# Optimization experiments

Measured on AMD Instinct MI355X. Metric: run time of the kernel, lower is better.

## Reference

```python
import jax, jax.numpy as jnp
import numpy as np
from functools import partial

N = 50000      # nodes
E = 800000     # edges
B = 64         # graphs in batch
D = 64         # embedding_dim (= per-head out_dim)
H = 2          # num_heads
G = 50         # n_gaussians
HID = 128      # hidden_dim of edge-filter net
MLP_DIM = 128  # mlp_dim of OutputMLP
OUT = 1        # output_dim
L = 3          # n_interactions
CUTOFF = 8.0
MEAN = 0.0
STD = 1.0


def ssp(x):
    # shifted softplus: softplus(x) - log(2)
    return jax.nn.softplus(x) - jnp.log(2.0)


def setup_inputs() -> dict:
    key = jax.random.key(0)
    ks = jax.random.split(key, 24)
    R = jax.random.normal(ks[0], (N, 3), dtype=jnp.float32) * 3.0
    Z = jax.random.randint(ks[1], (N,), 0, 100)
    src = jax.random.randint(ks[2], (E,), 0, N)
    dst = jax.random.randint(ks[3], (E,), 0, N)
    graph_ids = jnp.sort(jax.random.randint(ks[4], (N,), 0, B))
    # embedding table with padding_idx=0 zeroed
    emb_table = (jax.random.normal(ks[5], (100, D), dtype=jnp.float32) * 0.1).at[0].set(0.0)
    offsets = jnp.linspace(0.0, CUTOFF, G, dtype=jnp.float32)
    widths = jnp.full((G,), offsets[1] - offsets[0], dtype=jnp.float32)
    s = 0.1
    rn = lambda k, shp: jax.random.normal(k, shp, dtype=jnp.float32) * s
    return {
        "R": R, "Z": Z, "src": src, "dst": dst, "graph_ids": graph_ids,
        "emb_table": emb_table, "offsets": offsets, "widths": widths,
        "fc_w": rn(ks[6], (L, D, H * D)),
        "attn_l": rn(ks[7], (L, H, D)),
        "attn_r": rn(ks[8], (L, H, D)),
        "filt_w1": rn(ks[9], (L, G, HID)), "filt_b1": jnp.zeros((L, HID), jnp.float32),
        "filt_w2": rn(ks[10], (L, HID, H * D)), "filt_b2": jnp.zeros((L, H * D), jnp.float32),
        "mlp_w1": rn(ks[11], (L, H * D, D)), "mlp_b1": jnp.zeros((L, D), jnp.float32),
        "mlp_w2": rn(ks[12], (L, D, D)), "mlp_b2": jnp.zeros((L, D), jnp.float32),
        "out_w1": rn(ks[13], (D, MLP_DIM)), "out_b1": jnp.zeros((MLP_DIM,), jnp.float32),
        "out_w2": rn(ks[14], (MLP_DIM, OUT)), "out_b2": jnp.zeros((OUT,), jnp.float32),
    }


def _forward(R, emb_table, offsets, widths, fc_w, attn_l, attn_r,
             filt_w1, filt_b1, filt_w2, filt_b2,
             mlp_w1, mlp_b1, mlp_w2, mlp_b2,
             out_w1, out_b1, out_w2, out_b2,
             Z, src, dst, graph_ids):
    # per-edge distances
    r = jnp.linalg.norm(R[src] - R[dst], axis=1)  # (E,)
    # Gaussian smearing (trainable offsets/widths, schnetpack style)
    coeff = -0.5 / (widths ** 2)
    gs = jnp.exp(coeff * (r[:, None] - offsets) ** 2)  # (E, G)
    # cosine cutoff
    C = 0.5 * (jnp.cos(r * (jnp.pi / CUTOFF)) + 1.0) * (r < CUTOFF).astype(r.dtype)  # (E,)
    x = emb_table[Z]  # (N, D)
    for l in range(L):
        h = (x @ fc_w[l]).reshape(N, H, D)  # (N, H, D)
        # cfconv-style edge filter from gaussian features
        w = ssp(gs @ filt_w1[l] + filt_b1[l]) @ filt_w2[l] + filt_b2[l]  # (E, H*D)
        w = w.reshape(E, H, D)
        msg = h[src] * w * C[:, None, None]  # (E, H, D)
        # GAT attention, softmax over incoming edges per dst node
        el = jnp.einsum('nhd,hd->nh', h, attn_l[l])
        er = jnp.einsum('nhd,hd->nh', h, attn_r[l])
        e = jax.nn.leaky_relu(el[src] + er[dst], negative_slope=0.2)  # (E, H)
        m = jax.ops.segment_max(e, dst, num_segments=N)  # (N, H)
        ex = jnp.exp(e - m[dst])
        denom = jax.ops.segment_sum(ex, dst, num_segments=N)  # (N, H)
        alpha = ex / denom[dst]  # (E, H)
        agg = jax.ops.segment_sum(alpha[:, :, None] * msg, dst, num_segments=N)  # (N, H, D)
        v = ssp(agg).reshape(N, H * D)
        v = ssp(v @ mlp_w1[l] + mlp_b1[l]) @ mlp_w2[l] + mlp_b2[l]  # (N, D)
        x = x + v
    hh = ssp(x @ out_w1 + out_b1) @ out_w2 + out_b2  # (N, OUT)
    hh = hh * STD + MEAN
    return jax.ops.segment_sum(hh, graph_ids, num_segments=B)  # (B, OUT)


def reference(R, Z, src, dst, graph_ids, emb_table, offsets, widths,
              fc_w, attn_l, attn_r, filt_w1, filt_b1, filt_w2, filt_b2,
              mlp_w1, mlp_b1, mlp_w2, mlp_b2,
              out_w1, out_b1, out_w2, out_b2):
    return _forward(R, emb_table, offsets, widths, fc_w, attn_l, attn_r,
                    filt_w1, filt_b1, filt_w2, filt_b2,
                    mlp_w1, mlp_b1, mlp_w2, mlp_b2,
                    out_w1, out_b1, out_w2, out_b2,
                    Z, src, dst, graph_ids)
```

## Files before the change

kernel.cpp:

```cpp
#include <hip/hip_runtime.h>
#include <stdint.h>

#define N_NODES 50000
#define N_EDGES 800000
#define B_GRAPHS 64
#define D_DIM 64
#define HD 128
#define G_GAUSS 50
#define HID_DIM 128
#define L_LAYERS 3
#define LN2 0.69314718055994530942f
#define PI_OVER_8 0.39269908169872414f
#define NCHUNK 196

#define TN 64
#define TLD 132
#define XLD 68
#define NBLK ((N_NODES + TN - 1) / TN)

#define LUT_T 2048
#define LUT_ROWS (LUT_T + 1)
#define LROWS 8

__device__ __forceinline__ float sspf(float x) {
    float ax = fabsf(x);
    return fmaxf(x, 0.f) + __logf(1.f + __expf(-ax)) - LN2;
}
__device__ __forceinline__ unsigned short f2bf(float f) {
    union { float f; unsigned int i; } v; v.f = f;
    unsigned int u = v.i;
    return (unsigned short)((u + 0x7FFFu + ((u >> 16) & 1u)) >> 16);
}

__global__ void repr_prep(int* __restrict__ count, float* __restrict__ dout) {
    int i = blockIdx.x * 256 + threadIdx.x;
    if (i < N_NODES) count[i] = 0;
    else if (i < N_NODES + B_GRAPHS) dout[i - N_NODES] = 0.f;
}

#define ZTOT ((N_NODES * HD + 2 * N_NODES) / 4)
__global__ void repr_zero(float* __restrict__ agg, float* __restrict__ denom) {
    int i = blockIdx.x * 256 + threadIdx.x;
    float4 z = make_float4(0.f, 0.f, 0.f, 0.f);
    if (i < N_NODES * HD / 4) ((float4*)agg)[i] = z;
    else if (i < ZTOT) ((float4*)denom)[i - N_NODES * HD / 4] = z;
}

__global__ __launch_bounds__(256) void repr_lut_build(
    const float* __restrict__ offs, const float* __restrict__ widths,
    const float* __restrict__ fw1, const float* __restrict__ fb1,
    const float* __restrict__ fw2, const float* __restrict__ fb2,
    unsigned int* __restrict__ lut)
{
    __shared__ float gs_s[LROWS + 1][G_GAUSS];
    __shared__ float hid_s[LROWS + 1][HID_DIM];
    __shared__ float wc_s[LROWS + 1][HD];
    const int nb = LUT_T / LROWS;
    int l = blockIdx.x / nb;
    int i0r = (blockIdx.x % nb) * LROWS;
    int tid = threadIdx.x;
    const float step = 8.0f / LUT_T;

    for (int j = tid; j < (LROWS + 1) * G_GAUSS; j += 256) {
        int r = j / G_GAUSS, k = j - r * G_GAUSS;
        float rr = (i0r + r) * step;
        float wdt = widths[k];
        float dr = rr - offs[k];
        gs_s[r][k] = expf(-0.5f / (wdt * wdt) * dr * dr);
    }
    __syncthreads();

    int c = tid & 127, sub = tid >> 7;
    int rlo = sub * 4;
    {
        const float* W1 = fw1 + (size_t)l * G_GAUSS * HID_DIM + c;
        float acc[5];
        float bb = fb1[l * HID_DIM + c];
        #pragma unroll
        for (int r = 0; r < 5; r++) acc[r] = bb;
        for (int k = 0; k < G_GAUSS; k++) {
            float wv = W1[k * HID_DIM];
            #pragma unroll
            for (int r = 0; r < 5; r++)
                acc[r] = fmaf(gs_s[rlo + r][k], wv, acc[r]);
        }
        #pragma unroll
        for (int r = 0; r < 5; r++) hid_s[rlo + r][c] = sspf(acc[r]);
    }
    __syncthreads();
    {
        const float* W2 = fw2 + (size_t)l * HID_DIM * HD + c;
        float acc[5];
        float bb = fb2[l * HD + c];
        #pragma unroll
        for (int r = 0; r < 5; r++) acc[r] = bb;
        for (int k = 0; k < HID_DIM; k++) {
            float wv = W2[k * HD];
            #pragma unroll
            for (int r = 0; r < 5; r++)
                acc[r] = fmaf(hid_s[rlo + r][k], wv, acc[r]);
        }
        #pragma unroll
        for (int r = 0; r < 5; r++) {
            float rr = (i0r + rlo + r) * step;
            float C = (rr < 8.0f) ? 0.5f * (cosf(rr * PI_OVER_8) + 1.f) : 0.f;
            wc_s[rlo + r][c] = acc[r] * C;
        }
    }
    __syncthreads();
    for (int j = tid; j < LROWS * HD; j += 256) {
        int r = j >> 7, cc = j & 127;
        unsigned int lo = f2bf(wc_s[r][cc]);
        unsigned int hi = f2bf(wc_s[r + 1][cc]);
        lut[((size_t)l * LUT_ROWS + i0r + r) * HD + cc] = lo | (hi << 16);
    }
    if (i0r == LUT_T - LROWS && tid < HD)
        lut[((size_t)l * LUT_ROWS + LUT_T) * HD + tid] = 0u;
}

__global__ void repr_hist(const float* __restrict__ R,
                          const int* __restrict__ src, const int* __restrict__ dst,
                          int* __restrict__ count,
                          int2* __restrict__ pk) {
    int e = blockIdx.x * blockDim.x + threadIdx.x;
    if (e >= N_EDGES) return;
    int s = src[e], d = dst[e];
    float dx = R[3*s+0] - R[3*d+0];
    float dy = R[3*s+1] - R[3*d+1];
    float dz = R[3*s+2] - R[3*d+2];
    float r = sqrtf(dx*dx + dy*dy + dz*dz);
    unsigned rf = (r < 8.0f) ? (unsigned)(r * 16777216.f) : (2048u << 16);
    if (rf > (2048u << 16)) rf = 2048u << 16;
    pk[e] = make_int2((int)((unsigned)s | ((unsigned)d << 16)), (int)rf);
    atomicAdd(&count[d], 1);
}

__global__ void repr_scanA(const int* __restrict__ cnt, int* __restrict__ excl,
                           int* __restrict__ bsum) {
    __shared__ int tmp[256];
    int t = threadIdx.x, b = blockIdx.x;
    int i = b * 256 + t;
    int v = (i < N_NODES) ? cnt[i] : 0;
    tmp[t] = v; __syncthreads();
    for (int off = 1; off < 256; off <<= 1) {
        int add = (t >= off) ? tmp[t - off] : 0;
        __syncthreads();
        tmp[t] += add;
        __syncthreads();
    }
    if (i < N_NODES) excl[i] = tmp[t] - v;
    if (t == 255) bsum[b] = tmp[255];
}
__global__ void repr_scanB(const int* __restrict__ bsum, int* __restrict__ bpref) {
    __shared__ int tmp[256];
    int t = threadIdx.x;
    int v = (t < NCHUNK) ? bsum[t] : 0;
    tmp[t] = v; __syncthreads();
    for (int off = 1; off < 256; off <<= 1) {
        int add = (t >= off) ? tmp[t - off] : 0;
        __syncthreads();
        tmp[t] += add;
        __syncthreads();
    }
    if (t < NCHUNK) bpref[t] = tmp[t] - v;
}
__global__ void repr_scanC(const int* __restrict__ excl, const int* __restrict__ bpref,
                           int* __restrict__ cur) {
    int i = blockIdx.x * 256 + threadIdx.x;
    if (i < N_NODES) cur[i] = excl[i] + bpref[blockIdx.x];
}

__global__ void repr_scatter(const int2* __restrict__ pk,
                             int* __restrict__ cur,
                             int2* __restrict__ surv) {
    int e = blockIdx.x * blockDim.x + threadIdx.x;
    if (e >= N_EDGES) return;
    int2 v = pk[e];
    int d = (int)((unsigned)v.x >> 16);
    int pos = atomicAdd(&cur[d], 1);
    surv[pos] = v;
}


__device__ __forceinline__ void load_ssp_agg(int base, int tid,
        const float* __restrict__ agg, const float* __restrict__ denom,
        float* __restrict__ bufA) {
    int row = tid >> 2;
    int c0 = (tid & 3) << 5;
    int n = base + row;
    float2 dn = *(const float2*)&denom[2 * (size_t)n];
    float i0v = dn.x > 0.f ? 1.f / dn.x : 0.f;
    float i1v = dn.y > 0.f ? 1.f / dn.y : 0.f;
    float inv = (c0 < 64) ? i0v : i1v;
    const float* ap = agg + (size_t)n * HD + c0;
    float* tp = bufA + row * TLD + c0;
    #pragma unroll
    for (int j = 0; j < 8; j++) {
        float4 v = *(const float4*)(ap + j * 4);
        tp[j*4+0] = sspf(v.x * inv); tp[j*4+1] = sspf(v.y * inv);
        tp[j*4+2] = sspf(v.z * inv); tp[j*4+3] = sspf(v.w * inv);
    }
}

__device__ __forceinline__ void gemm_mlp(int base, int tid,
        const float* __restrict__ w1, const float* __restrict__ b1,
        const float* __restrict__ w2, const float* __restrict__ b2,
        float* __restrict__ x, float* __restrict__ bufA, float* __restrict__ v1s)
{
    const int rg = tid >> 4, cg = tid & 15;
    const int r0 = rg * 4, c0 = cg * 4;
    float acc[4][4];
    #pragma unroll
    for (int r = 0; r < 4; r++)
        #pragma unroll
        for (int c = 0; c < 4; c++) acc[r][c] = 0.f;
    for (int k0 = 0; k0 < 128; k0 += 4) {
        float av[4][4];
        #pragma unroll
        for (int r = 0; r < 4; r++)
            *(float4*)av[r] = *(const float4*)&bufA[(r0 + r) * TLD + k0];
        #pragma unroll
        for (int kk = 0; kk < 4; kk++) {
            float4 wv = *(const float4*)(w1 + (k0 + kk) * 64 + c0);
            float wf[4] = {wv.x, wv.y, wv.z, wv.w};
            #pragma unroll
            for (int r = 0; r < 4; r++)
                #pragma unroll
                for (int c = 0; c < 4; c++)
                    acc[r][c] = fmaf(av[r][kk], wf[c], acc[r][c]);
        }
    }
    {
        float4 bv = *(const float4*)(b1 + c0);
        float ba[4] = {bv.x, bv.y, bv.z, bv.w};
        #pragma unroll
        for (int r = 0; r < 4; r++)
            #pragma unroll
            for (int c = 0; c < 4; c++)
                v1s[(r0 + r) * XLD + c0 + c] = sspf(acc[r][c] + ba[c]);
    }
    __syncthreads();
    float acc2[4][4];
    #pragma unroll
    for (int r = 0; r < 4; r++)
        #pragma unroll
        for (int c = 0; c < 4; c++) acc2[r][c] = 0.f;
    for (int k0 = 0; k0 < 64; k0 += 4) {
        float av[4][4];
        #pragma unroll
        for (int r = 0; r < 4; r++)
            *(float4*)av[r] = *(const float4*)&v1s[(r0 + r) * XLD + k0];
        #pragma unroll
        for (int kk = 0; kk < 4; kk++) {
            float4 wv = *(const float4*)(w2 + (k0 + kk) * 64 + c0);
            float wf[4] = {wv.x, wv.y, wv.z, wv.w};
            #pragma unroll
            for (int r = 0; r < 4; r++)
                #pragma unroll
                for (int c = 0; c < 4; c++)
                    acc2[r][c] = fmaf(av[r][kk], wf[c], acc2[r][c]);
        }
    }
    {
        float4 bv = *(const float4*)(b2 + c0);
        #pragma unroll
        for (int r = 0; r < 4; r++) {
            int n = base + r0 + r;
            float4 xv = *(const float4*)(x + (size_t)n * 64 + c0);
            float4 o;
            o.x = acc2[r][0] + bv.x + xv.x;
            o.y = acc2[r][1] + bv.y + xv.y;
            o.z = acc2[r][2] + bv.z + xv.z;
            o.w = acc2[r][3] + bv.w + xv.w;
            *(float4*)&bufA[(r0 + r) * XLD + c0] = o;
            if (n < N_NODES) *(float4*)(x + (size_t)n * 64 + c0) = o;
        }
    }
    __syncthreads();
}

__device__ __forceinline__ void gemm_h(int base, int tid,
        const float* __restrict__ bufA,
        const float* __restrict__ fc_w, const float* __restrict__ attn_l,
        const float* __restrict__ attn_r,
        unsigned int* __restrict__ hq, float* __restrict__ el, float* __restrict__ er)
{
    const int rg = tid >> 4, cg = tid & 15;
    const int r0 = rg * 4, c0 = cg * 8;
    float acc[4][8];
    #pragma unroll
    for (int r = 0; r < 4; r++)
        #pragma unroll
        for (int c = 0; c < 8; c++) acc[r][c] = 0.f;
    for (int k0 = 0; k0 < 64; k0 += 4) {
        float av[4][4];
        #pragma unroll
        for (int r = 0; r < 4; r++)
            *(float4*)av[r] = *(const float4*)&bufA[(r0 + r) * XLD + k0];
        #pragma unroll
        for (int kk = 0; kk < 4; kk++) {
            float4 w0 = *(const float4*)(fc_w + (k0 + kk) * 128 + c0);
            float4 w1v = *(const float4*)(fc_w + (k0 + kk) * 128 + c0 + 4);
            float wf[8] = {w0.x, w0.y, w0.z, w0.w, w1v.x, w1v.y, w1v.z, w1v.w};
            #pragma unroll
            for (int r = 0; r < 4; r++)
                #pragma unroll
                for (int c = 0; c < 8; c++)
                    acc[r][c] = fmaf(av[r][kk], wf[c], acc[r][c]);
        }
    }
    float al[8], ar[8];
    #pragma unroll
    for (int c = 0; c < 8; c++) { al[c] = attn_l[c0 + c]; ar[c] = attn_r[c0 + c]; }
    int head = cg >> 3;
    #pragma unroll
    for (int r = 0; r < 4; r++) {
        int n = base + r0 + r;
        float pel = 0.f, per = 0.f;
        #pragma unroll
        for (int c = 0; c < 8; c++) {
            pel = fmaf(acc[r][c], al[c], pel);
            per = fmaf(acc[r][c], ar[c], per);
        }
        if (n < N_NODES) {
            uint4 pv;
            pv.x = (unsigned int)f2bf(acc[r][0]) | ((unsigned int)f2bf(acc[r][1]) << 16);
            pv.y = (unsigned int)f2bf(acc[r][2]) | ((unsigned int)f2bf(acc[r][3]) << 16);
            pv.z = (unsigned int)f2bf(acc[r][4]) | ((unsigned int)f2bf(acc[r][5]) << 16);
            pv.w = (unsigned int)f2bf(acc[r][6]) | ((unsigned int)f2bf(acc[r][7]) << 16);
            *(uint4*)(hq + (size_t)n * 64 + cg * 4) = pv;
        }
        #pragma unroll
        for (int off = 1; off < 8; off <<= 1) {
            pel += __shfl_xor(pel, off, 64);
            per += __shfl_xor(per, off, 64);
        }
        if ((cg & 7) == 0 && n < N_NODES) {
            el[n * 2 + head] = pel;
            er[n * 2 + head] = per;
        }
    }
}

__global__ __launch_bounds__(256) void repr_embed_h(
        const float* __restrict__ emb, const int* __restrict__ Z,
        const float* __restrict__ fc_w, const float* __restrict__ attn_l,
        const float* __restrict__ attn_r,
        float* __restrict__ x, unsigned int* __restrict__ hq,
        float* __restrict__ el, float* __restrict__ er) {
    __shared__ float bufA[TN * XLD];
    int base = blockIdx.x * TN, tid = threadIdx.x;
    int row = tid >> 2;
    int c0 = (tid & 3) << 4;
    int n = base + row;
    int z = (n < N_NODES) ? Z[n] : 0;
    const float* ep = emb + (size_t)z * D_DIM + c0;
    float* bp = bufA + row * XLD + c0;
    #pragma unroll
    for (int j = 0; j < 4; j++) {
        float4 v = *(const float4*)(ep + j * 4);
        *(float4*)(bp + j * 4) = v;
        if (n < N_NODES) *(float4*)(x + (size_t)n * D_DIM + c0 + j * 4) = v;
    }
    __syncthreads();
    gemm_h(base, tid, bufA, fc_w, attn_l, attn_r, hq, el, er);
}

__global__ __launch_bounds__(256) void repr_mlp_h(
        const float* __restrict__ agg, const float* __restrict__ denom,
        const float* __restrict__ w1, const float* __restrict__ b1,
        const float* __restrict__ w2, const float* __restrict__ b2,
        const float* __restrict__ fc_w, const float* __restrict__ attn_l,
        const float* __restrict__ attn_r,
        float* __restrict__ x, unsigned int* __restrict__ hq,
        float* __restrict__ el, float* __restrict__ er) {
    __shared__ float bufA[TN * TLD];
    __shared__ float v1s[TN * XLD];
    int base = blockIdx.x * TN, tid = threadIdx.x;
    load_ssp_agg(base, tid, agg, denom, bufA);
    __syncthreads();
    gemm_mlp(base, tid, w1, b1, w2, b2, x, bufA, v1s);
    gemm_h(base, tid, bufA, fc_w, attn_l, attn_r, hq, el, er);
}

__global__ __launch_bounds__(256) void repr_mlp_out(
        const float* __restrict__ agg, const float* __restrict__ denom,
        const float* __restrict__ w1, const float* __restrict__ b1,
        const float* __restrict__ w2, const float* __restrict__ b2,
        const float* __restrict__ ow1, const float* __restrict__ ob1,
        const float* __restrict__ ow2, const float* __restrict__ ob2,
        float* __restrict__ x, float* __restrict__ hh) {
    __shared__ float bufA[TN * TLD];
    __shared__ float v1s[TN * XLD];
    int base = blockIdx.x * TN, tid = threadIdx.x;
    load_ssp_agg(base, tid, agg, denom, bufA);
    __syncthreads();
    gemm_mlp(base, tid, w1, b1, w2, b2, x, bufA, v1s);
    const int rg = tid >> 4, cg = tid & 15;
    const int r0 = rg * 4, c0 = cg * 8;
    float acc[4][8];
    #pragma unroll
    for (int r = 0; r < 4; r++)
        #pragma unroll
        for (int c = 0; c < 8; c++) acc[r][c] = 0.f;
    for (int k0 = 0; k0 < 64; k0 += 4) {
        float av[4][4];
        #pragma unroll
        for (int r = 0; r < 4; r++)
            *(float4*)av[r] = *(const float4*)&bufA[(r0 + r) * XLD + k0];
        #pragma unroll
        for (int kk = 0; kk < 4; kk++) {
            float4 w0 = *(const float4*)(ow1 + (k0 + kk) * 128 + c0);
            float4 w1v = *(const float4*)(ow1 + (k0 + kk) * 128 + c0 + 4);
            float wf[8] = {w0.x, w0.y, w0.z, w0.w, w1v.x, w1v.y, w1v.z, w1v.w};
            #pragma unroll
            for (int r = 0; r < 4; r++)
                #pragma unroll
                for (int c = 0; c < 8; c++)
                    acc[r][c] = fmaf(av[r][kk], wf[c], acc[r][c]);
        }
    }
    float o1[8], w2c[8];
    #pragma unroll
    for (int c = 0; c < 8; c++) { o1[c] = ob1[c0 + c]; w2c[c] = ow2[c0 + c]; }
    #pragma unroll
    for (int r = 0; r < 4; r++) {
        int n = base + r0 + r;
        float s = 0.f;
        #pragma unroll
        for (int c = 0; c < 8; c++)
            s = fmaf(sspf(acc[r][c] + o1[c]), w2c[c], s);
        #pragma unroll
        for (int off = 1; off < 16; off <<= 1)
            s += __shfl_xor(s, off, 64);
        if (cg == 0 && n < N_NODES) hh[n] = s + ob2[0];
    }
}

#define TILE 64
__global__ __launch_bounds__(256) void repr_msg_lut(
    const int2* __restrict__ surv,
    const float* __restrict__ el, const float* __restrict__ er,
    const unsigned int* __restrict__ hq,
    const unsigned int* __restrict__ lut,
    float* __restrict__ agg, float* __restrict__ denom)
{
    __shared__ int4 rowinfo[TILE];
    __shared__ float scl[TILE][2];
    int base = blockIdx.x * TILE;
    int tid = threadIdx.x;
    int d_own = -1; float e0 = 0.f, e1 = 0.f;
    if (tid < TILE) {
        int2 ev = surv[base + tid];
        int sn = (int)((unsigned)ev.x & 0xFFFFu);
        d_own  = (int)((unsigned)ev.x >> 16);
        unsigned rf = (unsigned)ev.y;
        int i0 = (int)(rf >> 16);
        float fr = (float)(rf & 0xFFFFu) * (1.f / 65536.f);
        float2 a = *(const float2*)&el[2 * sn];
        float2 b = *(const float2*)&er[2 * d_own];
        float v0 = a.x + b.x; v0 = v0 >= 0.f ? v0 : 0.2f * v0;
        float v1 = a.y + b.y; v1 = v1 >= 0.f ? v1 : 0.2f * v1;
        e0 = __expf(v0); e1 = __expf(v1);
        rowinfo[tid] = make_int4(i0, sn, d_own, __float_as_int(fr));
        scl[tid][0] = e0; scl[tid][1] = e1;
    }
    __syncthreads();
    if (tid < TILE) {
        int dprev = __shfl_up(d_own, 1, 64);
        bool headl = (tid == 0) || (d_own != dprev);
        if (headl) {
            float s0 = e0, s1 = e1;
            for (int r = tid + 1; r < TILE; r++) {
                if (rowinfo[r].z != d_own) break;
                s0 += scl[r][0]; s1 += scl[r][1];
            }
            atomicAdd(&denom[2 * d_own], s0);
            atomicAdd(&denom[2 * d_own + 1], s1);
        }
    }
    const int cp = tid & 63;
    const int sp = tid >> 6;
    const int head = cp >> 5;
    const int lo = sp * 16;
    const uint2* __restrict__ l2p = (const uint2*)lut;
    float sum0 = 0.f, sum1 = 0.f;
    int cur_d = -1;
    int seg_first = 1;
    #pragma unroll 4
    for (int j = 0; j < 16; j++) {
        int r = lo + j;
        int4 ri = rowinfo[r];
        if (ri.z != cur_d) {
            if (cur_d >= 0) {
                float* ap = &agg[(size_t)cur_d * HD + 2 * cp];
                if (seg_first) { atomicAdd(ap, sum0); atomicAdd(ap + 1, sum1); }
                else *(float2*)ap = make_float2(sum0, sum1);
            }
            cur_d = ri.z; sum0 = 0.f; sum1 = 0.f; seg_first = (j == 0);
        }
        uint2 tv = l2p[(size_t)ri.x * 64 + cp];
        float fr = __int_as_float(ri.w);
        float wa0 = __uint_as_float(tv.x << 16);
        float wa1 = __uint_as_float(tv.x & 0xFFFF0000u);
        float wb0 = __uint_as_float(tv.y << 16);
        float wb1 = __uint_as_float(tv.y & 0xFFFF0000u);
        unsigned int hv = hq[(size_t)ri.y * 64 + cp];
        float ha = __uint_as_float(hv << 16);
        float hb = __uint_as_float(hv & 0xFFFF0000u);
        float s = scl[r][head];
        float wa = fmaf(fr, wa1 - wa0, wa0);
        float wb = fmaf(fr, wb1 - wb0, wb0);
        sum0 = fmaf(wa * ha, s, sum0);
        sum1 = fmaf(wb * hb, s, sum1);
    }
    if (cur_d >= 0) {
        float* ap = &agg[(size_t)cur_d * HD + 2 * cp];
        atomicAdd(ap, sum0); atomicAdd(ap + 1, sum1);
    }
}

__global__ void repr_gsum(const float* __restrict__ hh, const int* __restrict__ gids,
                          float* __restrict__ dout) {
    __shared__ float bins[B_GRAPHS];
    int t = threadIdx.x;
    if (t < B_GRAPHS) bins[t] = 0.f;
    __syncthreads();
    int i = blockIdx.x * 256 + t;
    if (i < N_NODES) atomicAdd(&bins[gids[i]], hh[i]);
    __syncthreads();
    if (t < B_GRAPHS && bins[t] != 0.f) atomicAdd(&dout[t], bins[t]);
}

extern "C" void kernel_launch(void* const* d_in, const int* in_sizes, int n_in,
                              void* d_out, int out_size, void* d_ws, size_t ws_size,
                              hipStream_t stream) {
    (void)in_sizes; (void)n_in; (void)out_size; (void)ws_size;
    const float* R      = (const float*)d_in[0];
    const int*   Z      = (const int*)d_in[1];
    const int*   src    = (const int*)d_in[2];
    const int*   dst    = (const int*)d_in[3];
    const int*   gids   = (const int*)d_in[4];
    const float* emb    = (const float*)d_in[5];
    const float* offs   = (const float*)d_in[6];
    const float* widths = (const float*)d_in[7];
    const float* fc_w   = (const float*)d_in[8];
    const float* attn_l = (const float*)d_in[9];
    const float* attn_r = (const float*)d_in[10];
    const float* fw1    = (const float*)d_in[11];
    const float* fb1    = (const float*)d_in[12];
    const float* fw2    = (const float*)d_in[13];
    const float* fb2    = (const float*)d_in[14];
    const float* mw1    = (const float*)d_in[15];
    const float* mb1    = (const float*)d_in[16];
    const float* mw2    = (const float*)d_in[17];
    const float* mb2    = (const float*)d_in[18];
    const float* ow1    = (const float*)d_in[19];
    const float* ob1    = (const float*)d_in[20];
    const float* ow2    = (const float*)d_in[21];
    const float* ob2    = (const float*)d_in[22];

    char* p = (char*)d_ws;
    float* x      = (float*)p; p += (size_t)N_NODES * 64 * 4;
    unsigned int* hq = (unsigned int*)p; p += (size_t)N_NODES * 64 * 4;
    float* el     = (float*)p; p += (size_t)N_NODES * 2 * 4;
    float* er     = (float*)p; p += (size_t)N_NODES * 2 * 4;
    float* denom  = (float*)p; p += (size_t)N_NODES * 2 * 4;
    float* agg    = (float*)p; p += (size_t)N_NODES * 128 * 4;
    int2*  surv   = (int2*)p;  p += (size_t)N_EDGES * 8;
    int2*  pk     = (int2*)p;  p += (size_t)N_EDGES * 8;
    float* hh     = (float*)p; p += (size_t)N_NODES * 4;
    int*   bsum   = (int*)p;   p += 1024;
    int*   bpref  = (int*)p;   p += 1024;
    unsigned int* lut = (unsigned int*)pk;
    int* count = (int*)x;
    int* excl  = (int*)((char*)x + 256 * 1024);
    int* cur   = (int*)((char*)x + 512 * 1024);

    repr_prep<<<(N_NODES + B_GRAPHS + 255) / 256, 256, 0, stream>>>(
        count, (float*)d_out);
    repr_hist<<<N_EDGES / 256, 256, 0, stream>>>(R, src, dst, count, pk);
    repr_scanA<<<NCHUNK, 256, 0, stream>>>(count, excl, bsum);
    repr_scanB<<<1, 256, 0, stream>>>(bsum, bpref);
    repr_scanC<<<NCHUNK, 256, 0, stream>>>(excl, bpref, cur);
    repr_scatter<<<N_EDGES / 256, 256, 0, stream>>>(pk, cur, surv);

    repr_lut_build<<<L_LAYERS * (LUT_T / LROWS), 256, 0, stream>>>(
        offs, widths, fw1, fb1, fw2, fb2, lut);

    repr_embed_h<<<NBLK, 256, 0, stream>>>(
        emb, Z, fc_w, attn_l, attn_r, x, hq, el, er);

    for (int l = 0; l < L_LAYERS; l++) {
        repr_zero<<<(ZTOT + 255) / 256, 256, 0, stream>>>(agg, denom);
        repr_msg_lut<<<N_EDGES / TILE, 256, 0, stream>>>(
            surv, el, er, hq, lut + (size_t)l * LUT_ROWS * HD, agg, denom);
        if (l < L_LAYERS - 1) {
            repr_mlp_h<<<NBLK, 256, 0, stream>>>(
                agg, denom, mw1 + (size_t)l * 128 * 64, mb1 + l * 64,
                mw2 + (size_t)l * 64 * 64, mb2 + l * 64,
                fc_w + (size_t)(l + 1) * 64 * 128, attn_l + (l + 1) * 128,
                attn_r + (l + 1) * 128, x, hq, el, er);
        } else {
            repr_mlp_out<<<NBLK, 256, 0, stream>>>(
                agg, denom, mw1 + (size_t)l * 128 * 64, mb1 + l * 64,
                mw2 + (size_t)l * 64 * 64, mb2 + l * 64,
                ow1, ob1, ow2, ob2, x, hh);
        }
    }
    repr_gsum<<<NCHUNK, 256, 0, stream>>>(hh, gids, (float*)d_out);
}
```

Before: 689.6 us.

## Aggregate messages per destination node via CSR rowptr instead of edge tiles

Builds a CSR row pointer from the existing prefix scan and replaces the edge-tiled message kernel with a node-centric kernel. Each block handles 8 destination nodes, with four wave slices striding over each node's incoming edges. Partial sums are reduced in shared memory and written out once per node. This removes the per-layer zeroing kernel and the global atomics on agg and denom, at the cost of load imbalance from variable node degree and serial edge loops.

Measured after the change: 852.9 us. 1.24x slower.

```diff
diff --git a/kernel.cpp b/kernel.cpp
--- a/kernel.cpp
+++ b/kernel.cpp
@@ -36,14 +36,6 @@
     int i = blockIdx.x * 256 + threadIdx.x;
     if (i < N_NODES) count[i] = 0;
     else if (i < N_NODES + B_GRAPHS) dout[i - N_NODES] = 0.f;
-}
-
-#define ZTOT ((N_NODES * HD + 2 * N_NODES) / 4)
-__global__ void repr_zero(float* __restrict__ agg, float* __restrict__ denom) {
-    int i = blockIdx.x * 256 + threadIdx.x;
-    float4 z = make_float4(0.f, 0.f, 0.f, 0.f);
-    if (i < N_NODES * HD / 4) ((float4*)agg)[i] = z;
-    else if (i < ZTOT) ((float4*)denom)[i - N_NODES * HD / 4] = z;
 }
 
 __global__ __launch_bounds__(256) void repr_lut_build(
@@ -165,9 +157,10 @@
     if (t < NCHUNK) bpref[t] = tmp[t] - v;
 }
 __global__ void repr_scanC(const int* __restrict__ excl, const int* __restrict__ bpref,
-                           int* __restrict__ cur) {
+                           int* __restrict__ cur, int* __restrict__ rowptr) {
     int i = blockIdx.x * 256 + threadIdx.x;
-    if (i < N_NODES) cur[i] = excl[i] + bpref[blockIdx.x];
+    if (i < N_NODES) { int v = excl[i] + bpref[blockIdx.x]; cur[i] = v; rowptr[i] = v; }
+    if (i == 0) rowptr[N_NODES] = N_EDGES;
 }
 
 __global__ void repr_scatter(const int2* __restrict__ pk,
@@ -437,87 +430,68 @@
     }
 }
 
-#define TILE 64
-__global__ __launch_bounds__(256) void repr_msg_lut(
-    const int2* __restrict__ surv,
+#define DN 8
+__global__ __launch_bounds__(256) void repr_msg_node(
+    const int2* __restrict__ surv, const int* __restrict__ rowptr,
     const float* __restrict__ el, const float* __restrict__ er,
     const unsigned int* __restrict__ hq,
     const unsigned int* __restrict__ lut,
     float* __restrict__ agg, float* __restrict__ denom)
 {
-    __shared__ int4 rowinfo[TILE];
-    __shared__ float scl[TILE][2];
-    int base = blockIdx.x * TILE;
+    __shared__ float lagg[DN][HD];
+    __shared__ float lden[DN][2];
     int tid = threadIdx.x;
-    int d_own = -1; float e0 = 0.f, e1 = 0.f;
-    if (tid < TILE) {
-        int2 ev = surv[base + tid];
-        int sn = (int)((unsigned)ev.x & 0xFFFFu);
-        d_own  = (int)((unsigned)ev.x >> 16);
-        unsigned rf = (unsigned)ev.y;
-        int i0 = (int)(rf >> 16);
-        float fr = (float)(rf & 0xFFFFu) * (1.f / 65536.f);
-        float2 a = *(const float2*)&el[2 * sn];
-        float2 b = *(const float2*)&er[2 * d_own];
-        float v0 = a.x + b.x; v0 = v0 >= 0.f ? v0 : 0.2f * v0;
-        float v1 = a.y + b.y; v1 = v1 >= 0.f ? v1 : 0.2f * v1;
-        e0 = __expf(v0); e1 = __expf(v1);
-        rowinfo[tid] = make_int4(i0, sn, d_own, __float_as_int(fr));
-        scl[tid][0] = e0; scl[tid][1] = e1;
-    }
-    __syncthreads();
-    if (tid < TILE) {
-        int dprev = __shfl_up(d_own, 1, 64);
-        bool headl = (tid == 0) || (d_own != dprev);
-        if (headl) {
-            float s0 = e0, s1 = e1;
-            for (int r = tid + 1; r < TILE; r++) {
-                if (rowinfo[r].z != d_own) break;
-                s0 += scl[r][0]; s1 += scl[r][1];
-            }
-            atomicAdd(&denom[2 * d_own], s0);
-            atomicAdd(&denom[2 * d_own + 1], s1);
-        }
-    }
-    const int cp = tid & 63;
-    const int sp = tid >> 6;
-    const int head = cp >> 5;
-    const int lo = sp * 16;
+    int cp = tid & 63, slice = tid >> 6;
+    int d0 = blockIdx.x * DN;
+    ((float4*)lagg)[tid] = make_float4(0.f, 0.f, 0.f, 0.f);
+    if (tid < DN * 2) ((float*)lden)[tid] = 0.f;
+    __syncthreads();
+
     const uint2* __restrict__ l2p = (const uint2*)lut;
-    float sum0 = 0.f, sum1 = 0.f;
-    int cur_d = -1;
-    int seg_first = 1;
-    #pragma unroll 4
-    for (int j = 0; j < 16; j++) {
-        int r = lo + j;
-        int4 ri = rowinfo[r];
-        if (ri.z != cur_d) {
-            if (cur_d >= 0) {
-                float* ap = &agg[(size_t)cur_d * HD + 2 * cp];
-                if (seg_first) { atomicAdd(ap, sum0); atomicAdd(ap + 1, sum1); }
-                else *(float2*)ap = make_float2(sum0, sum1);
-            }
-            cur_d = ri.z; sum0 = 0.f; sum1 = 0.f; seg_first = (j == 0);
-        }
-        uint2 tv = l2p[(size_t)ri.x * 64 + cp];
-        float fr = __int_as_float(ri.w);
-        float wa0 = __uint_as_float(tv.x << 16);
-        float wa1 = __uint_as_float(tv.x & 0xFFFF0000u);
-        float wb0 = __uint_as_float(tv.y << 16);
-        float wb1 = __uint_as_float(tv.y & 0xFFFF0000u);
-        unsigned int hv = hq[(size_t)ri.y * 64 + cp];
-        float ha = __uint_as_float(hv << 16);
-        float hb = __uint_as_float(hv & 0xFFFF0000u);
-        float s = scl[r][head];
-        float wa = fmaf(fr, wa1 - wa0, wa0);
-        float wb = fmaf(fr, wb1 - wb0, wb0);
-        sum0 = fmaf(wa * ha, s, sum0);
-        sum1 = fmaf(wb * hb, s, sum1);
-    }
-    if (cur_d >= 0) {
-        float* ap = &agg[(size_t)cur_d * HD + 2 * cp];
-        atomicAdd(ap, sum0); atomicAdd(ap + 1, sum1);
-    }
+    for (int dd = 0; dd < DN; dd++) {
+        int d = d0 + dd;
+        int rs = rowptr[d];
+        int re = rowptr[d + 1];
+        if (rs + slice >= re) continue;
+        float2 b = *(const float2*)&er[2 * d];
+        float acc0 = 0.f, acc1 = 0.f, den0 = 0.f, den1 = 0.f;
+        for (int i = rs + slice; i < re; i += 4) {
+            int2 ev = surv[i];
+            int sn = (int)((unsigned)ev.x & 0xFFFFu);
+            unsigned rf = (unsigned)ev.y;
+            int i0 = (int)(rf >> 16);
+            float fr = (float)(rf & 0xFFFFu) * (1.f / 65536.f);
+            float2 a = *(const float2*)&el[2 * sn];
+            float v0 = a.x + b.x; v0 = v0 >= 0.f ? v0 : 0.2f * v0;
+            float v1 = a.y + b.y; v1 = v1 >= 0.f ? v1 : 0.2f * v1;
+            float e0 = __expf(v0), e1 = __expf(v1);
+            den0 += e0; den1 += e1;
+            uint2 tv = l2p[(size_t)i0 * 64 + cp];
+            unsigned int hv = hq[(size_t)sn * 64 + cp];
+            float wa0 = __uint_as_float(tv.x << 16);
+            float wa1 = __uint_as_float(tv.x & 0xFFFF0000u);
+            float wb0 = __uint_as_float(tv.y << 16);
+            float wb1 = __uint_as_float(tv.y & 0xFFFF0000u);
+            float ha = __uint_as_float(hv << 16);
+            float hb = __uint_as_float(hv & 0xFFFF0000u);
+            float s = (cp < 32) ? e0 : e1;
+            float wa = fmaf(fr, wa1 - wa0, wa0);
+            float wb = fmaf(fr, wb1 - wb0, wb0);
+            acc0 = fmaf(wa * ha, s, acc0);
+            acc1 = fmaf(wb * hb, s, acc1);
+        }
+        atomicAdd(&lagg[dd][2 * cp], acc0);
+        atomicAdd(&lagg[dd][2 * cp + 1], acc1);
+        if (cp == 0) {
+            atomicAdd(&lden[dd][0], den0);
+            atomicAdd(&lden[dd][1], den1);
+        }
+    }
+    __syncthreads();
+    int node = tid >> 5;
+    int c4 = (tid & 31) * 4;
+    *(float4*)&agg[(size_t)(d0 + node) * HD + c4] = *(float4*)&lagg[node][c4];
+    if (tid < DN * 2) denom[2 * d0 + tid] = ((float*)lden)[tid];
 }
 
 __global__ void repr_gsum(const float* __restrict__ hh, const int* __restrict__ gids,
@@ -569,6 +543,7 @@
     float* agg    = (float*)p; p += (size_t)N_NODES * 128 * 4;
     int2*  surv   = (int2*)p;  p += (size_t)N_EDGES * 8;
     int2*  pk     = (int2*)p;  p += (size_t)N_EDGES * 8;
+    int*   rowptr = (int*)p;   p += (size_t)(N_NODES + 1) * 4;
     float* hh     = (float*)p; p += (size_t)N_NODES * 4;
     int*   bsum   = (int*)p;   p += 1024;
     int*   bpref  = (int*)p;   p += 1024;
@@ -582,7 +557,7 @@
     repr_hist<<<N_EDGES / 256, 256, 0, stream>>>(R, src, dst, count, pk);
     repr_scanA<<<NCHUNK, 256, 0, stream>>>(count, excl, bsum);
     repr_scanB<<<1, 256, 0, stream>>>(bsum, bpref);
-    repr_scanC<<<NCHUNK, 256, 0, stream>>>(excl, bpref, cur);
+    repr_scanC<<<NCHUNK, 256, 0, stream>>>(excl, bpref, cur, rowptr);
     repr_scatter<<<N_EDGES / 256, 256, 0, stream>>>(pk, cur, surv);
 
     repr_lut_build<<<L_LAYERS * (LUT_T / LROWS), 256, 0, stream>>>(
@@ -592,9 +567,8 @@
         emb, Z, fc_w, attn_l, attn_r, x, hq, el, er);
 
     for (int l = 0; l < L_LAYERS; l++) {
-        repr_zero<<<(ZTOT + 255) / 256, 256, 0, stream>>>(agg, denom);
-        repr_msg_lut<<<N_EDGES / TILE, 256, 0, stream>>>(
-            surv, el, er, hq, lut + (size_t)l * LUT_ROWS * HD, agg, denom);
+        repr_msg_node<<<N_NODES / DN, 256, 0, stream>>>(
+            surv, rowptr, el, er, hq, lut + (size_t)l * LUT_ROWS * HD, agg, denom);
         if (l < L_LAYERS - 1) {
             repr_mlp_h<<<NBLK, 256, 0, stream>>>(
                 agg, denom, mw1 + (size_t)l * 128 * 64, mb1 + l * 64,
```

## Precompute softmax denominators per node via CSR pass and fuse agg zeroing

Applied to the files above, without the earlier changes.

Adds a CSR row pointer from the existing scan and a new per-destination kernel that computes the reciprocal softmax denominator from el/er before message passing. The same kernel also zeroes the agg rows, which replaces the separate zero kernel. The message kernel then scales each edge weight by the precomputed reciprocal, so the per-tile denominator segment reduction and its atomics go away, as does the per-node normalization in the MLP load. The cost is an extra pass over edges that gathers el and recomputes exp, and the per-node loop is irregular with 16 lanes per node.

Result: no change. 687.6 us (-0.3%).

```diff
diff --git a/kernel.cpp b/kernel.cpp
--- a/kernel.cpp
+++ b/kernel.cpp
@@ -36,14 +36,6 @@
     int i = blockIdx.x * 256 + threadIdx.x;
     if (i < N_NODES) count[i] = 0;
     else if (i < N_NODES + B_GRAPHS) dout[i - N_NODES] = 0.f;
-}
-
-#define ZTOT ((N_NODES * HD + 2 * N_NODES) / 4)
-__global__ void repr_zero(float* __restrict__ agg, float* __restrict__ denom) {
-    int i = blockIdx.x * 256 + threadIdx.x;
-    float4 z = make_float4(0.f, 0.f, 0.f, 0.f);
-    if (i < N_NODES * HD / 4) ((float4*)agg)[i] = z;
-    else if (i < ZTOT) ((float4*)denom)[i - N_NODES * HD / 4] = z;
 }
 
 __global__ __launch_bounds__(256) void repr_lut_build(
@@ -165,9 +157,10 @@
     if (t < NCHUNK) bpref[t] = tmp[t] - v;
 }
 __global__ void repr_scanC(const int* __restrict__ excl, const int* __restrict__ bpref,
-                           int* __restrict__ cur) {
+                           int* __restrict__ cur, int* __restrict__ rowptr) {
     int i = blockIdx.x * 256 + threadIdx.x;
-    if (i < N_NODES) cur[i] = excl[i] + bpref[blockIdx.x];
+    if (i < N_NODES) { int v = excl[i] + bpref[blockIdx.x]; cur[i] = v; rowptr[i] = v; }
+    if (i == 0) rowptr[N_NODES] = N_EDGES;
 }
 
 __global__ void repr_scatter(const int2* __restrict__ pk,
@@ -183,22 +176,16 @@
 
 
 __device__ __forceinline__ void load_ssp_agg(int base, int tid,
-        const float* __restrict__ agg, const float* __restrict__ denom,
-        float* __restrict__ bufA) {
+        const float* __restrict__ agg, float* __restrict__ bufA) {
     int row = tid >> 2;
     int c0 = (tid & 3) << 5;
-    int n = base + row;
-    float2 dn = *(const float2*)&denom[2 * (size_t)n];
-    float i0v = dn.x > 0.f ? 1.f / dn.x : 0.f;
-    float i1v = dn.y > 0.f ? 1.f / dn.y : 0.f;
-    float inv = (c0 < 64) ? i0v : i1v;
-    const float* ap = agg + (size_t)n * HD + c0;
+    const float* ap = agg + (size_t)(base + row) * HD + c0;
     float* tp = bufA + row * TLD + c0;
     #pragma unroll
     for (int j = 0; j < 8; j++) {
         float4 v = *(const float4*)(ap + j * 4);
-        tp[j*4+0] = sspf(v.x * inv); tp[j*4+1] = sspf(v.y * inv);
-        tp[j*4+2] = sspf(v.z * inv); tp[j*4+3] = sspf(v.w * inv);
+        tp[j*4+0] = sspf(v.x); tp[j*4+1] = sspf(v.y);
+        tp[j*4+2] = sspf(v.z); tp[j*4+3] = sspf(v.w);
     }
 }
 
@@ -367,7 +354,7 @@
 }
 
 __global__ __launch_bounds__(256) void repr_mlp_h(
-        const float* __restrict__ agg, const float* __restrict__ denom,
+        const float* __restrict__ agg,
         const float* __restrict__ w1, const float* __restrict__ b1,
         const float* __restrict__ w2, const float* __restrict__ b2,
         const float* __restrict__ fc_w, const float* __restrict__ attn_l,
@@ -377,14 +364,14 @@
     __shared__ float bufA[TN * TLD];
     __shared__ float v1s[TN * XLD];
     int base = blockIdx.x * TN, tid = threadIdx.x;
-    load_ssp_agg(base, tid, agg, denom, bufA);
+    load_ssp_agg(base, tid, agg, bufA);
     __syncthreads();
     gemm_mlp(base, tid, w1, b1, w2, b2, x, bufA, v1s);
     gemm_h(base, tid, bufA, fc_w, attn_l, attn_r, hq, el, er);
 }
 
 __global__ __launch_bounds__(256) void repr_mlp_out(
-        const float* __restrict__ agg, const float* __restrict__ denom,
+        const float* __restrict__ agg,
         const float* __restrict__ w1, const float* __restrict__ b1,
         const float* __restrict__ w2, const float* __restrict__ b2,
         const float* __restrict__ ow1, const float* __restrict__ ob1,
@@ -393,7 +380,7 @@
     __shared__ float bufA[TN * TLD];
     __shared__ float v1s[TN * XLD];
     int base = blockIdx.x * TN, tid = threadIdx.x;
-    load_ssp_agg(base, tid, agg, denom, bufA);
+    load_ssp_agg(base, tid, agg, bufA);
     __syncthreads();
     gemm_mlp(base, tid, w1, b1, w2, b2, x, bufA, v1s);
     const int rg = tid >> 4, cg = tid & 15;
@@ -437,48 +424,67 @@
     }
 }
 
+__global__ void repr_alpha(const int2* __restrict__ surv, const int* __restrict__ rowptr,
+                           const float* __restrict__ el, const float* __restrict__ er,
+                           float2* __restrict__ md, float* __restrict__ agg) {
+    int t = blockIdx.x * 256 + threadIdx.x;
+    int d = t >> 4;
+    int lane16 = t & 15;
+    if (d >= N_NODES) return;
+    float4 z = make_float4(0.f, 0.f, 0.f, 0.f);
+    float4* ar = (float4*)(agg + (size_t)d * HD);
+    ar[lane16 * 2] = z;
+    ar[lane16 * 2 + 1] = z;
+    int rs = rowptr[d];
+    int re = rowptr[d + 1];
+    float2 erd = *(const float2*)&er[2 * d];
+    float s0 = 0.f, s1 = 0.f;
+    for (int i = rs + lane16; i < re; i += 16) {
+        int s = (int)((unsigned)surv[i].x & 0xFFFFu);
+        float2 a = *(const float2*)&el[2 * s];
+        float v0 = a.x + erd.x; v0 = v0 >= 0.f ? v0 : 0.2f * v0;
+        float v1 = a.y + erd.y; v1 = v1 >= 0.f ? v1 : 0.2f * v1;
+        s0 += __expf(v0);
+        s1 += __expf(v1);
+    }
+    #pragma unroll
+    for (int off = 8; off > 0; off >>= 1) {
+        s0 += __shfl_xor(s0, off, 64);
+        s1 += __shfl_xor(s1, off, 64);
+    }
+    if (lane16 == 0) md[d] = make_float2(1.f / s0, 1.f / s1);
+}
+
 #define TILE 64
 __global__ __launch_bounds__(256) void repr_msg_lut(
     const int2* __restrict__ surv,
     const float* __restrict__ el, const float* __restrict__ er,
-    const unsigned int* __restrict__ hq,
+    const float2* __restrict__ md, const unsigned int* __restrict__ hq,
     const unsigned int* __restrict__ lut,
-    float* __restrict__ agg, float* __restrict__ denom)
+    float* __restrict__ agg)
 {
     __shared__ int4 rowinfo[TILE];
     __shared__ float scl[TILE][2];
     int base = blockIdx.x * TILE;
     int tid = threadIdx.x;
-    int d_own = -1; float e0 = 0.f, e1 = 0.f;
     if (tid < TILE) {
         int2 ev = surv[base + tid];
         int sn = (int)((unsigned)ev.x & 0xFFFFu);
-        d_own  = (int)((unsigned)ev.x >> 16);
+        int d  = (int)((unsigned)ev.x >> 16);
         unsigned rf = (unsigned)ev.y;
         int i0 = (int)(rf >> 16);
         float fr = (float)(rf & 0xFFFFu) * (1.f / 65536.f);
         float2 a = *(const float2*)&el[2 * sn];
-        float2 b = *(const float2*)&er[2 * d_own];
+        float2 b = *(const float2*)&er[2 * d];
+        float2 rd = md[d];
         float v0 = a.x + b.x; v0 = v0 >= 0.f ? v0 : 0.2f * v0;
         float v1 = a.y + b.y; v1 = v1 >= 0.f ? v1 : 0.2f * v1;
-        e0 = __expf(v0); e1 = __expf(v1);
-        rowinfo[tid] = make_int4(i0, sn, d_own, __float_as_int(fr));
-        scl[tid][0] = e0; scl[tid][1] = e1;
-    }
-    __syncthreads();
-    if (tid < TILE) {
-        int dprev = __shfl_up(d_own, 1, 64);
-        bool headl = (tid == 0) || (d_own != dprev);
-        if (headl) {
-            float s0 = e0, s1 = e1;
-            for (int r = tid + 1; r < TILE; r++) {
-                if (rowinfo[r].z != d_own) break;
-                s0 += scl[r][0]; s1 += scl[r][1];
-            }
-            atomicAdd(&denom[2 * d_own], s0);
-            atomicAdd(&denom[2 * d_own + 1], s1);
-        }
-    }
+        float sc0 = __expf(v0) * rd.x;
+        float sc1 = __expf(v1) * rd.y;
+        rowinfo[tid] = make_int4(i0, sn, d, __float_as_int(fr));
+        scl[tid][0] = sc0; scl[tid][1] = sc1;
+    }
+    __syncthreads();
     const int cp = tid & 63;
     const int sp = tid >> 6;
     const int head = cp >> 5;
@@ -565,10 +571,11 @@
     unsigned int* hq = (unsigned int*)p; p += (size_t)N_NODES * 64 * 4;
     float* el     = (float*)p; p += (size_t)N_NODES * 2 * 4;
     float* er     = (float*)p; p += (size_t)N_NODES * 2 * 4;
-    float* denom  = (float*)p; p += (size_t)N_NODES * 2 * 4;
+    float2* md    = (float2*)p; p += (size_t)N_NODES * 8;
     float* agg    = (float*)p; p += (size_t)N_NODES * 128 * 4;
     int2*  surv   = (int2*)p;  p += (size_t)N_EDGES * 8;
     int2*  pk     = (int2*)p;  p += (size_t)N_EDGES * 8;
+    int*   rowptr = (int*)p;   p += (size_t)(N_NODES + 1) * 4;
     float* hh     = (float*)p; p += (size_t)N_NODES * 4;
     int*   bsum   = (int*)p;   p += 1024;
     int*   bpref  = (int*)p;   p += 1024;
@@ -582,7 +589,7 @@
     repr_hist<<<N_EDGES / 256, 256, 0, stream>>>(R, src, dst, count, pk);
     repr_scanA<<<NCHUNK, 256, 0, stream>>>(count, excl, bsum);
     repr_scanB<<<1, 256, 0, stream>>>(bsum, bpref);
-    repr_scanC<<<NCHUNK, 256, 0, stream>>>(excl, bpref, cur);
+    repr_scanC<<<NCHUNK, 256, 0, stream>>>(excl, bpref, cur, rowptr);
     repr_scatter<<<N_EDGES / 256, 256, 0, stream>>>(pk, cur, surv);
 
     repr_lut_build<<<L_LAYERS * (LUT_T / LROWS), 256, 0, stream>>>(
@@ -592,18 +599,19 @@
         emb, Z, fc_w, attn_l, attn_r, x, hq, el, er);
 
     for (int l = 0; l < L_LAYERS; l++) {
-        repr_zero<<<(ZTOT + 255) / 256, 256, 0, stream>>>(agg, denom);
+        repr_alpha<<<(N_NODES * 16 + 255) / 256, 256, 0, stream>>>(
+            surv, rowptr, el, er, md, agg);
         repr_msg_lut<<<N_EDGES / TILE, 256, 0, stream>>>(
-            surv, el, er, hq, lut + (size_t)l * LUT_ROWS * HD, agg, denom);
+            surv, el, er, md, hq, lut + (size_t)l * LUT_ROWS * HD, agg);
         if (l < L_LAYERS - 1) {
             repr_mlp_h<<<NBLK, 256, 0, stream>>>(
-                agg, denom, mw1 + (size_t)l * 128 * 64, mb1 + l * 64,
+                agg, mw1 + (size_t)l * 128 * 64, mb1 + l * 64,
                 mw2 + (size_t)l * 64 * 64, mb2 + l * 64,
                 fc_w + (size_t)(l + 1) * 64 * 128, attn_l + (l + 1) * 128,
                 attn_r + (l + 1) * 128, x, hq, el, er);
         } else {
             repr_mlp_out<<<NBLK, 256, 0, stream>>>(
-                agg, denom, mw1 + (size_t)l * 128 * 64, mb1 + l * 64,
+                agg, mw1 + (size_t)l * 128 * 64, mb1 + l * 64,
                 mw2 + (size_t)l * 64 * 64, mb2 + l * 64,
                 ow1, ob1, ow2, ob2, x, hh);
         }
```
